# Kernel tuning notes

Hardware: AMD Instinct MI355X
Metric: run time of the kernel (lower is better)

Reference implementation:

```python
import jax, jax.numpy as jnp
import numpy as np
import math

D_MODEL = 2048
NUM_HEADS = 16
HEAD_DIM = D_MODEL // NUM_HEADS  # 128
B, S = 2, 2048


def setup_inputs() -> dict:
    key = jax.random.key(0)
    ks = jax.random.split(key, 11)
    s_in = 1.0 / math.sqrt(D_MODEL)
    return {
        "query": jax.random.normal(ks[0], (B, S, D_MODEL), dtype=jnp.float32),
        "key": jax.random.normal(ks[1], (B, S, D_MODEL), dtype=jnp.float32),
        "value": jax.random.normal(ks[2], (B, S, D_MODEL), dtype=jnp.float32),
        "Wq": jax.random.normal(ks[3], (D_MODEL, D_MODEL), dtype=jnp.float32) * s_in,
        "bq": jnp.zeros((D_MODEL,), dtype=jnp.float32),
        "Wk": jax.random.normal(ks[4], (D_MODEL, HEAD_DIM), dtype=jnp.float32) * s_in,
        "bk": jnp.zeros((HEAD_DIM,), dtype=jnp.float32),
        "Wv": jax.random.normal(ks[5], (D_MODEL, HEAD_DIM), dtype=jnp.float32) * s_in,
        "bv": jnp.zeros((HEAD_DIM,), dtype=jnp.float32),
        "Wo": jax.random.normal(ks[6], (D_MODEL, D_MODEL), dtype=jnp.float32) * s_in,
        "bo": jnp.zeros((D_MODEL,), dtype=jnp.float32),
    }


def reference(query, key, value, Wq, bq, Wk, bk, Wv, bv, Wo, bo):
    b, s, d_model = query.shape
    h, d = NUM_HEADS, HEAD_DIM
    # Projections: Q has h heads, K/V have a single shared head (MQA)
    Q = (query @ Wq + bq).reshape(b, s, h, d).transpose(0, 2, 1, 3)  # [b,h,s,d]
    K = key @ Wk + bk      # [b,s,d]
    V = value @ Wv + bv    # [b,s,d]
    scale = 1.0 / math.sqrt(d)
    # broadcast single K head over all h query heads
    scores = jnp.einsum('bhqd,bkd->bhqk', Q, K) * scale  # [b,h,s,s]
    weights = jax.nn.softmax(scores, axis=-1)
    attn = jnp.einsum('bhqk,bkd->bhqd', weights, V)      # [b,h,s,d]
    attn = attn.transpose(0, 2, 1, 3).reshape(b, s, d_model)
    return attn @ Wo + bo
```

## Files before the change

### kernel.cpp

```cpp
#include <hip/hip_runtime.h>


typedef unsigned short u16;
typedef __attribute__((ext_vector_type(8))) short bf16x8;
typedef __attribute__((ext_vector_type(4))) short bf16x4;
typedef __attribute__((ext_vector_type(4))) float f32x4;

#define D_MODEL 2048
#define SEQ     2048
#define NH      16
#define HD      128
#define BK      32

__device__ __forceinline__ u16 f2bf(float f){
  union { float f; unsigned u; } v; v.f = f;
  unsigned r = (v.u + 0x7FFFu + ((v.u >> 16) & 1u)) >> 16;
  return (u16)r;
}

#if __has_builtin(__builtin_amdgcn_cvt_pk_bf16_f32)
__device__ __forceinline__ unsigned pack2bf(float a, float b){
  auto v = __builtin_amdgcn_cvt_pk_bf16_f32(a, b);
  unsigned u; __builtin_memcpy(&u, &v, 4); return u;
}
#else
__device__ __forceinline__ unsigned pack2bf(float a, float b){
  return (unsigned)f2bf(a) | ((unsigned)f2bf(b) << 16);
}
#endif

__device__ __forceinline__ void gll16(const void* g, void* l){
  __builtin_amdgcn_global_load_lds(
      (const __attribute__((address_space(1))) void*)g,
      (__attribute__((address_space(3))) void*)l, 16, 0, 0);
}

__global__ __launch_bounds__(256) void prep_kernel(
    const float4* __restrict__ qa, const float4* __restrict__ ka, const float4* __restrict__ va,
    ushort4* __restrict__ oq, ushort4* __restrict__ ok, ushort4* __restrict__ ov,
    const float* __restrict__ Wq, const float* __restrict__ Wo,
    const float* __restrict__ Wk, const float* __restrict__ Wv,
    u16* __restrict__ WqT, u16* __restrict__ WoT,
    u16* __restrict__ WkT, u16* __restrict__ WvT){
  __shared__ float tt[32][33];
  int bid = blockIdx.x;
  if (bid < 8192){
    int i = bid*256 + threadIdx.x;
    float4 a = qa[i], b = ka[i], c = va[i];
    ushort4 ra, rb, rc;
    ra.x=f2bf(a.x); ra.y=f2bf(a.y); ra.z=f2bf(a.z); ra.w=f2bf(a.w);
    rb.x=f2bf(b.x); rb.y=f2bf(b.y); rb.z=f2bf(b.z); rb.w=f2bf(b.w);
    rc.x=f2bf(c.x); rc.y=f2bf(c.y); rc.z=f2bf(c.z); rc.w=f2bf(c.w);
    oq[i]=ra; ok[i]=rb; ov[i]=rc;
    return;
  }
  int id = bid - 8192;
  const float* in; u16* outp; int C, bx, by;
  if (id < 4096)      { in=Wq; outp=WqT; C=2048; bx=id&63;        by=id>>6; }
  else if (id < 8192) { id-=4096; in=Wo; outp=WoT; C=2048; bx=id&63; by=id>>6; }
  else if (id < 8448) { id-=8192; in=Wk; outp=WkT; C=128;  bx=id&3;  by=id>>2; }
  else                { id-=8448; in=Wv; outp=WvT; C=128;  bx=id&3;  by=id>>2; }
  const int R = 2048;
  int c0 = bx*32, r0 = by*32;
  int tx = threadIdx.x & 31, ty = threadIdx.x >> 5;
  #pragma unroll
  for (int k=0;k<4;k++) tt[ty+k*8][tx] = in[(size_t)(r0+ty+k*8)*C + c0+tx];
  __syncthreads();
  #pragma unroll
  for (int k=0;k<4;k++) outp[(size_t)(c0+ty+k*8)*R + r0+tx] = f2bf(tt[tx][ty+k*8]);
}

__device__ __forceinline__ void gemm_core_3p(
    const u16* __restrict__ A, const u16* __restrict__ BT,
    int lda, int ldb, int m0, int n0, int kbeg, int kend,
    u16* As, u16* Bs, f32x4 acc[4][4])
{
  const int t = threadIdx.x;
  const int w = t >> 6, l = t & 63;
  const int wr = w >> 1, wc = w & 1;
  const int c16 = l & 15, q = l >> 4;
  const int srow = l >> 2;
  const int sc   = ((l & 3) ^ ((l >> 3) & 3)) * 8;

  int aoff[4], boff[4];
  #pragma unroll
  for (int mt=0;mt<4;mt++){
    int row = wr*64 + mt*16 + c16;
    aoff[mt] = row*BK + ((q ^ ((row>>1)&3))*8);
  }
  #pragma unroll
  for (int nt=0;nt<4;nt++){
    int row = wc*64 + nt*16 + c16;
    boff[nt] = row*BK + ((q ^ ((row>>1)&3))*8);
  }

  auto issue = [&](int k0, int buf){
    u16* Ad = As + buf*4096;
    u16* Bd = Bs + buf*4096;
    #pragma unroll
    for (int half=0; half<2; half++){
      int r = half*64 + w*16 + srow;
      gll16(A  + (size_t)(m0+r)*lda + k0 + sc, Ad + (half*64 + w*16)*BK);
      gll16(BT + (size_t)(n0+r)*ldb + k0 + sc, Bd + (half*64 + w*16)*BK);
    }
  };

  const int n = (kend - kbeg) / BK;
  issue(kbeg, 0);
  issue(kbeg + BK, 1);
  int bi = 0;
  for (int i = 0; i < n; i++){
    if (i + 1 < n) asm volatile("s_waitcnt vmcnt(4)" ::: "memory");
    else           asm volatile("s_waitcnt vmcnt(0)" ::: "memory");
    __builtin_amdgcn_s_barrier();
    if (i + 2 < n){
      int nb = bi + 2; if (nb >= 3) nb -= 3;
      issue(kbeg + (i+2)*BK, nb);
    }
    const u16* Ab = As + bi*4096;
    const u16* Bb = Bs + bi*4096;
    bf16x8 af[4], bfr[4];
    #pragma unroll
    for (int mt=0;mt<4;mt++) af[mt]  = *(const bf16x8*)(Ab + aoff[mt]);
    #pragma unroll
    for (int nt=0;nt<4;nt++) bfr[nt] = *(const bf16x8*)(Bb + boff[nt]);
    #pragma unroll
    for (int mt=0;mt<4;mt++)
      #pragma unroll
      for (int nt=0;nt<4;nt++)
        acc[mt][nt] = __builtin_amdgcn_mfma_f32_16x16x32_bf16(af[mt], bfr[nt], acc[mt][nt], 0,0,0);
    bi++; if (bi == 3) bi = 0;
  }
}

__global__ __launch_bounds__(256) void proj_kernel(
    const u16* __restrict__ qb, const u16* __restrict__ kb, const u16* __restrict__ vb,
    const u16* __restrict__ WqT, const u16* __restrict__ WkT, const u16* __restrict__ WvT,
    const float* __restrict__ bq, u16* __restrict__ Qp, float* __restrict__ part)
{
  __shared__ u16 As[3*4096], Bs[3*4096];
  f32x4 acc[4][4];
  f32x4 z = {0.f,0.f,0.f,0.f};
  #pragma unroll
  for (int i=0;i<4;i++) for (int j=0;j<4;j++) acc[i][j] = z;
  const int t = threadIdx.x, w = t>>6, l = t&63, wr = w>>1, wc = w&1, c16 = l&15, q = l>>4;
  int id = blockIdx.x;
  if (id < 512){
    int x = id & 7, j = id >> 3;
    int m0 = (x*4 + (j & 3))*128, n0 = (j >> 2)*128;
    gemm_core_3p(qb, WqT, 2048, 2048, m0, n0, 0, 2048, As, Bs, acc);
    #pragma unroll
    for (int mt=0;mt<4;mt++)
      #pragma unroll
      for (int nt=0;nt<4;nt++){
        int col = n0 + wc*64 + nt*16 + c16;
        float bv = bq[col];
        #pragma unroll
        for (int r=0;r<4;r++){
          int row = m0 + wr*64 + mt*16 + q*4 + r;
          Qp[(size_t)row*D_MODEL + col] = f2bf(acc[mt][nt][r] + bv);
        }
      }
  } else {
    int kvid = id - 512;
    int zi = kvid & 3, nb = (kvid >> 2) & 1, mi = kvid >> 3;
    const u16* Am = nb ? vb  : kb;
    const u16* Bm = nb ? WvT : WkT;
    gemm_core_3p(Am, Bm, 2048, 2048, mi*128, 0, zi*512, zi*512+512, As, Bs, acc);
    float* dst = part + (size_t)(zi*2 + nb)*524288;
    #pragma unroll
    for (int mt=0;mt<4;mt++)
      #pragma unroll
      for (int nt=0;nt<4;nt++){
        int col = wc*64 + nt*16 + c16;
        #pragma unroll
        for (int r=0;r<4;r++){
          int row = mi*128 + wr*64 + mt*16 + q*4 + r;
          dst[(size_t)row*128 + col] = acc[mt][nt][r];
        }
      }
  }
}

__global__ __launch_bounds__(256) void oproj_kernel(
    const u16* __restrict__ A, const u16* __restrict__ BT, const float* __restrict__ bias,
    float* __restrict__ C)
{
  __shared__ u16 As[3*4096], Bs[3*4096];
  f32x4 acc[4][4];
  f32x4 z = {0.f,0.f,0.f,0.f};
  #pragma unroll
  for (int i=0;i<4;i++) for (int j=0;j<4;j++) acc[i][j] = z;
  int id = blockIdx.x;
  int x = id & 7, j = id >> 3;
  int m0 = (x*4 + (j & 3))*128, n0 = (j >> 2)*128;
  gemm_core_3p(A, BT, 2048, 2048, m0, n0, 0, 2048, As, Bs, acc);
  const int t = threadIdx.x, w = t>>6, l = t&63, wr = w>>1, wc = w&1, c16 = l&15, q = l>>4;
  #pragma unroll
  for (int mt=0;mt<4;mt++)
    #pragma unroll
    for (int nt=0;nt<4;nt++){
      int col = n0 + wc*64 + nt*16 + c16;
      float bv = bias[col];
      #pragma unroll
      for (int r=0;r<4;r++){
        int row = m0 + wr*64 + mt*16 + q*4 + r;
        C[(size_t)row*D_MODEL + col] = acc[mt][nt][r] + bv;
      }
    }
}

__global__ __launch_bounds__(256) void kv_reduce_kernel(
    const float* __restrict__ part, const float* __restrict__ bk, const float* __restrict__ bv,
    u16* __restrict__ Kp, u16* __restrict__ VpT){
  int idx = blockIdx.x*256 + threadIdx.x;
  int d = idx & 127, sg = idx >> 7;
  float ka = 0.f, va = 0.f;
  #pragma unroll
  for (int zi=0; zi<4; zi++){
    ka += part[(size_t)(zi*2+0)*524288 + idx];
    va += part[(size_t)(zi*2+1)*524288 + idx];
  }
  Kp[idx] = f2bf(ka + bk[d]);
  int b = sg >> 11, sl = sg & 2047;
  VpT[(size_t)b*262144 + (size_t)d*2048 + sl] = f2bf(va + bv[d]);
}

__global__ __launch_bounds__(512, 2) void attn_kernel(
    const u16* __restrict__ Qp, const u16* __restrict__ Kp,
    const u16* __restrict__ VpT, u16* __restrict__ attnb){
  __shared__ u16 lds[65536];
  const int t = threadIdx.x;
  const int w = t >> 6, l = t & 63;
  const int c16 = l & 15, q = l >> 4;

  const int qt = blockIdx.x;
  const int bh = blockIdx.y;
  const int b = bh >> 4, h = bh & 15;

  const u16* Qbase = Qp  + ((size_t)(b*SEQ + qt*256 + w*32))*D_MODEL + h*HD;
  const u16* Kbase = Kp  + (size_t)(b*SEQ)*HD;
  const u16* Vbase = VpT + (size_t)b*HD*SEQ;

  const int sr = w*4 + (l >> 4);
  #pragma unroll
  for (int j=0;j<4;j++){
    int r = j*32 + sr;
    int g = (l & 15) ^ (r & 15);
    gll16(Kbase + (size_t)r*HD + g*8, lds + j*4096 + w*512);
  }
  #pragma unroll
  for (int j=0;j<4;j++){
    int d = j*32 + sr;
    int g = (l & 15) ^ (d & 15);
    gll16(Vbase + (size_t)d*SEQ + g*8, lds + 32768 + j*4096 + w*512);
  }
  bf16x8 qf[2][4];
  #pragma unroll
  for (int qs=0;qs<2;qs++)
    #pragma unroll
    for (int kk=0;kk<4;kk++)
      qf[qs][kk] = *(const bf16x8*)(Qbase + (size_t)(qs*16 + c16)*D_MODEL + (kk*4 + q)*8);
  __syncthreads();

  f32x4 o[2][8];
  f32x4 z4 = {0.f,0.f,0.f,0.f};
  #pragma unroll
  for (int qs=0;qs<2;qs++) for (int dt=0;dt<8;dt++) o[qs][dt] = z4;
  float mrow[2] = {-1e30f, -1e30f};
  float lrow[2] = {0.f, 0.f};
  const float cs = 0.08838834764831845f * 1.4426950408889634f;

  for (int kt = 0; kt < 16; kt++){
    const int p = kt & 1;
    if (kt < 15){
      u16* Kd = lds + (p^1)*16384;
      u16* Vd = lds + 32768 + (p^1)*16384;
      #pragma unroll
      for (int j=0;j<4;j++){
        int r = j*32 + sr;
        int g = (l & 15) ^ (r & 15);
        gll16(Kbase + (size_t)((kt+1)*128 + r)*HD + g*8, Kd + j*4096 + w*512);
      }
      #pragma unroll
      for (int j=0;j<4;j++){
        int d = j*32 + sr;
        int g = (l & 15) ^ (d & 15);
        gll16(Vbase + (size_t)d*SEQ + (kt+1)*128 + g*8, Vd + j*4096 + w*512);
      }
    }
    const u16* Ks = lds + p*16384;
    const u16* Vs = lds + 32768 + p*16384;

    f32x4 s[2][8];
    __builtin_amdgcn_s_setprio(1);
    #pragma unroll
    for (int kt8=0; kt8<8; kt8++){
      {
        bf16x8 kf = *(const bf16x8*)(Ks + (kt8*16 + c16)*128 + ((q ^ c16) & 15)*8);
        s[0][kt8] = __builtin_amdgcn_mfma_f32_16x16x32_bf16(kf, qf[0][0], z4, 0,0,0);
        s[1][kt8] = __builtin_amdgcn_mfma_f32_16x16x32_bf16(kf, qf[1][0], z4, 0,0,0);
      }
      #pragma unroll
      for (int kk=1;kk<4;kk++){
        int ch = kk*4 + q;
        bf16x8 kf = *(const bf16x8*)(Ks + (kt8*16 + c16)*128 + ((ch ^ c16) & 15)*8);
        s[0][kt8] = __builtin_amdgcn_mfma_f32_16x16x32_bf16(kf, qf[0][kk], s[0][kt8], 0,0,0);
        s[1][kt8] = __builtin_amdgcn_mfma_f32_16x16x32_bf16(kf, qf[1][kk], s[1][kt8], 0,0,0);
      }
    }
    __builtin_amdgcn_s_setprio(0);

    float vmax[2];
    #pragma unroll
    for (int qs=0; qs<2; qs++){
      float xx[8];
      #pragma unroll
      for (int kt8=0;kt8<8;kt8++)
        xx[kt8] = fmaxf(fmaxf(s[qs][kt8][0],s[qs][kt8][1]), fmaxf(s[qs][kt8][2],s[qs][kt8][3]));
      float vm = fmaxf(fmaxf(fmaxf(xx[0],xx[1]),fmaxf(xx[2],xx[3])),
                       fmaxf(fmaxf(xx[4],xx[5]),fmaxf(xx[6],xx[7])));
      vm = fmaxf(vm, __shfl_xor(vm, 16));
      vm = fmaxf(vm, __shfl_xor(vm, 32));
      vmax[qs] = vm;
    }
    bool upd = ((vmax[0]-mrow[0])*cs > 8.f) || ((vmax[1]-mrow[1])*cs > 8.f);
    if (__any(upd)){
      #pragma unroll
      for (int qs=0; qs<2; qs++){
        float mnew = fmaxf(mrow[qs], vmax[qs]);
        float a = exp2f((mrow[qs]-mnew)*cs);
        mrow[qs] = mnew; lrow[qs] *= a;
        #pragma unroll
        for (int dt=0;dt<8;dt++)
          #pragma unroll
          for (int r=0;r<4;r++) o[qs][dt][r] *= a;
      }
    }
    union PU { unsigned u[4]; bf16x8 v; } P32[2][4];
    #pragma unroll
    for (int qs=0; qs<2; qs++){
      float mc = mrow[qs]*cs;
      float rsum = 0.f;
      #pragma unroll
      for (int kt8=0;kt8<8;kt8++){
        float p0 = exp2f(__builtin_fmaf(s[qs][kt8][0], cs, -mc));
        float p1 = exp2f(__builtin_fmaf(s[qs][kt8][1], cs, -mc));
        float p2 = exp2f(__builtin_fmaf(s[qs][kt8][2], cs, -mc));
        float p3 = exp2f(__builtin_fmaf(s[qs][kt8][3], cs, -mc));
        s[qs][kt8][0]=p0; s[qs][kt8][1]=p1; s[qs][kt8][2]=p2; s[qs][kt8][3]=p3;
        rsum += (p0+p1)+(p2+p3);
      }
      rsum += __shfl_xor(rsum, 16);
      rsum += __shfl_xor(rsum, 32);
      lrow[qs] += rsum;
      #pragma unroll
      for (int kb=0;kb<4;kb++){
        P32[qs][kb].u[0] = pack2bf(s[qs][2*kb][0],   s[qs][2*kb][1]);
        P32[qs][kb].u[1] = pack2bf(s[qs][2*kb][2],   s[qs][2*kb][3]);
        P32[qs][kb].u[2] = pack2bf(s[qs][2*kb+1][0], s[qs][2*kb+1][1]);
        P32[qs][kb].u[3] = pack2bf(s[qs][2*kb+1][2], s[qs][2*kb+1][3]);
      }
    }

    __builtin_amdgcn_s_setprio(1);
    #pragma unroll
    for (int kb=0; kb<4; kb++){
      int ca = 4*kb + (q>>1);
      int cb = ca + 2;
      #pragma unroll
      for (int dt=0; dt<8; dt++){
        int d = dt*16 + c16;
        union VU { bf16x4 hh[2]; bf16x8 v; } vf;
        vf.hh[0] = *(const bf16x4*)(Vs + d*128 + ((ca ^ c16) & 15)*8 + (q&1)*4);
        vf.hh[1] = *(const bf16x4*)(Vs + d*128 + ((cb ^ c16) & 15)*8 + (q&1)*4);
        o[0][dt] = __builtin_amdgcn_mfma_f32_16x16x32_bf16(vf.v, P32[0][kb].v, o[0][dt], 0,0,0);
        o[1][dt] = __builtin_amdgcn_mfma_f32_16x16x32_bf16(vf.v, P32[1][kb].v, o[1][dt], 0,0,0);
      }
    }
    __builtin_amdgcn_s_setprio(0);
    __syncthreads();
  }

  #pragma unroll
  for (int qs=0;qs<2;qs++){
    float inv = 1.f / lrow[qs];
    int qrow = qt*256 + w*32 + qs*16 + c16;
    u16* dst = attnb + ((size_t)(b*SEQ) + qrow)*D_MODEL + h*HD + q*4;
    #pragma unroll
    for (int dt=0;dt<8;dt++){
      ushort4 pk;
      pk.x = f2bf(o[qs][dt][0]*inv);
      pk.y = f2bf(o[qs][dt][1]*inv);
      pk.z = f2bf(o[qs][dt][2]*inv);
      pk.w = f2bf(o[qs][dt][3]*inv);
      *(ushort4*)(dst + dt*16) = pk;
    }
  }
}

extern "C" void kernel_launch(void* const* d_in, const int* in_sizes, int n_in,
                              void* d_out, int out_size, void* d_ws, size_t ws_size,
                              hipStream_t stream) {
  (void)in_sizes; (void)n_in; (void)out_size; (void)ws_size;
  const float* query = (const float*)d_in[0];
  const float* key   = (const float*)d_in[1];
  const float* value = (const float*)d_in[2];
  const float* Wq    = (const float*)d_in[3];
  const float* bq    = (const float*)d_in[4];
  const float* Wk    = (const float*)d_in[5];
  const float* bk    = (const float*)d_in[6];
  const float* Wv    = (const float*)d_in[7];
  const float* bv    = (const float*)d_in[8];
  const float* Wo    = (const float*)d_in[9];
  const float* bo    = (const float*)d_in[10];
  float* out = (float*)d_out;

  char* W = (char*)d_ws;
  u16*  qb     = (u16*) (W + 0);
  u16*  kb     = (u16*) (W + 16777216);
  u16*  vb     = (u16*) (W + 33554432);
  u16*  WqT    = (u16*) (W + 50331648);
  u16*  WoT    = (u16*) (W + 58720256);
  u16*  WkT    = (u16*) (W + 67108864);
  u16*  WvT    = (u16*) (W + 67633152);
  u16*  Qp     = (u16*) (W + 68157440);
  u16*  Kp     = (u16*) (W + 84934656);
  u16*  VpT    = (u16*) (W + 85983232);
  u16*  attnb  = (u16*) (W + 87031808);
  float* kvpart= (float*)(W + 103809024);

  prep_kernel<<<16896, 256, 0, stream>>>(
      (const float4*)query, (const float4*)key, (const float4*)value,
      (ushort4*)qb, (ushort4*)kb, (ushort4*)vb,
      Wq, Wo, Wk, Wv, WqT, WoT, WkT, WvT);
  proj_kernel<<<768, 256, 0, stream>>>(qb, kb, vb, WqT, WkT, WvT, bq, Qp, kvpart);
  kv_reduce_kernel<<<2048, 256, 0, stream>>>(kvpart, bk, bv, Kp, VpT);
  attn_kernel<<<dim3(8,32), 512, 0, stream>>>(Qp, Kp, VpT, attnb);
  oproj_kernel<<<512, 256, 0, stream>>>(attnb, WoT, bo, out);
}
```

Measured before the change: 404.3 us.

## Fuse Q projection into attention kernel prologue

Moves the Q projection GEMM out of proj_kernel and computes each 256x128 Q tile inside attn_kernel, staging it through LDS before the flash-attention loop. This removes the Qp global round-trip and the separate Q tiles in the projection launch. In exchange, the attention blocks do a full K=2048 GEMM prologue with only 256 blocks of 512 threads, which may lower GEMM efficiency versus the wider 512-block projection launch.

Measured after the change: 385.7 us. 4.6% less time.

```diff
diff --git a/kernel.cpp b/kernel.cpp
--- a/kernel.cpp
+++ b/kernel.cpp
@@ -134,9 +134,9 @@
 }
 
 __global__ __launch_bounds__(256) void proj_kernel(
-    const u16* __restrict__ qb, const u16* __restrict__ kb, const u16* __restrict__ vb,
-    const u16* __restrict__ WqT, const u16* __restrict__ WkT, const u16* __restrict__ WvT,
-    const float* __restrict__ bq, u16* __restrict__ Qp, float* __restrict__ part)
+    const u16* __restrict__ kb, const u16* __restrict__ vb,
+    const u16* __restrict__ WkT, const u16* __restrict__ WvT,
+    float* __restrict__ part)
 {
   __shared__ u16 As[3*4096], Bs[3*4096];
   f32x4 acc[4][4];
@@ -145,41 +145,22 @@
   for (int i=0;i<4;i++) for (int j=0;j<4;j++) acc[i][j] = z;
   const int t = threadIdx.x, w = t>>6, l = t&63, wr = w>>1, wc = w&1, c16 = l&15, q = l>>4;
   int id = blockIdx.x;
-  if (id < 512){
-    int x = id & 7, j = id >> 3;
-    int m0 = (x*4 + (j & 3))*128, n0 = (j >> 2)*128;
-    gemm_core_3p(qb, WqT, 2048, 2048, m0, n0, 0, 2048, As, Bs, acc);
-    #pragma unroll
-    for (int mt=0;mt<4;mt++)
-      #pragma unroll
-      for (int nt=0;nt<4;nt++){
-        int col = n0 + wc*64 + nt*16 + c16;
-        float bv = bq[col];
-        #pragma unroll
-        for (int r=0;r<4;r++){
-          int row = m0 + wr*64 + mt*16 + q*4 + r;
-          Qp[(size_t)row*D_MODEL + col] = f2bf(acc[mt][nt][r] + bv);
-        }
-      }
-  } else {
-    int kvid = id - 512;
-    int zi = kvid & 3, nb = (kvid >> 2) & 1, mi = kvid >> 3;
-    const u16* Am = nb ? vb  : kb;
-    const u16* Bm = nb ? WvT : WkT;
-    gemm_core_3p(Am, Bm, 2048, 2048, mi*128, 0, zi*512, zi*512+512, As, Bs, acc);
-    float* dst = part + (size_t)(zi*2 + nb)*524288;
-    #pragma unroll
-    for (int mt=0;mt<4;mt++)
-      #pragma unroll
-      for (int nt=0;nt<4;nt++){
-        int col = wc*64 + nt*16 + c16;
-        #pragma unroll
-        for (int r=0;r<4;r++){
-          int row = mi*128 + wr*64 + mt*16 + q*4 + r;
-          dst[(size_t)row*128 + col] = acc[mt][nt][r];
-        }
-      }
-  }
+  int zi = id & 3, nb = (id >> 2) & 1, mi = id >> 3;
+  const u16* Am = nb ? vb  : kb;
+  const u16* Bm = nb ? WvT : WkT;
+  gemm_core_3p(Am, Bm, 2048, 2048, mi*128, 0, zi*512, zi*512+512, As, Bs, acc);
+  float* dst = part + (size_t)(zi*2 + nb)*524288;
+  #pragma unroll
+  for (int mt=0;mt<4;mt++)
+    #pragma unroll
+    for (int nt=0;nt<4;nt++){
+      int col = wc*64 + nt*16 + c16;
+      #pragma unroll
+      for (int r=0;r<4;r++){
+        int row = mi*128 + wr*64 + mt*16 + q*4 + r;
+        dst[(size_t)row*128 + col] = acc[mt][nt][r];
+      }
+    }
 }
 
 __global__ __launch_bounds__(256) void oproj_kernel(
@@ -227,8 +208,8 @@
 }
 
 __global__ __launch_bounds__(512, 2) void attn_kernel(
-    const u16* __restrict__ Qp, const u16* __restrict__ Kp,
-    const u16* __restrict__ VpT, u16* __restrict__ attnb){
+    const u16* __restrict__ qb, const u16* __restrict__ WqT, const float* __restrict__ bq,
+    const u16* __restrict__ Kp, const u16* __restrict__ VpT, u16* __restrict__ attnb){
   __shared__ u16 lds[65536];
   const int t = threadIdx.x;
   const int w = t >> 6, l = t & 63;
@@ -238,10 +219,89 @@
   const int bh = blockIdx.y;
   const int b = bh >> 4, h = bh & 15;
 
-  const u16* Qbase = Qp  + ((size_t)(b*SEQ + qt*256 + w*32))*D_MODEL + h*HD;
+  f32x4 o[2][8];
+  f32x4 z4 = {0.f,0.f,0.f,0.f};
+  #pragma unroll
+  for (int qs=0;qs<2;qs++) for (int dt=0;dt<8;dt++) o[qs][dt] = z4;
+
+  {
+    const u16* Aq = qb  + (size_t)(b*SEQ + qt*256)*D_MODEL;
+    const u16* Bw = WqT + (size_t)(h*HD)*D_MODEL;
+    u16* As = lds;
+    u16* Bs = lds + 24576;
+    const int srow = l >> 2;
+    const int sc   = ((l & 3) ^ ((l >> 3) & 3)) * 8;
+    auto issueQ = [&](int k0, int buf){
+      u16* Ad = As + buf*8192;
+      u16* Bd = Bs + buf*4096;
+      #pragma unroll
+      for (int half=0; half<2; half++){
+        int r = half*128 + w*16 + srow;
+        gll16(Aq + (size_t)r*D_MODEL + k0 + sc, Ad + (half*128 + w*16)*BK);
+      }
+      { int r = w*16 + srow;
+        gll16(Bw + (size_t)r*D_MODEL + k0 + sc, Bd + (w*16)*BK); }
+    };
+    issueQ(0, 0);
+    issueQ(BK, 1);
+    int bi = 0;
+    const int swz = (q ^ ((c16>>1)&3))*8;
+    for (int i = 0; i < 64; i++){
+      if (i + 1 < 64) asm volatile("s_waitcnt vmcnt(3)" ::: "memory");
+      else            asm volatile("s_waitcnt vmcnt(0)" ::: "memory");
+      __builtin_amdgcn_s_barrier();
+      if (i + 2 < 64){
+        int nb2 = bi + 2; if (nb2 >= 3) nb2 -= 3;
+        issueQ((i+2)*BK, nb2);
+      }
+      const u16* Ab = As + bi*8192;
+      const u16* Bb = Bs + bi*4096;
+      bf16x8 qrow0 = *(const bf16x8*)(Ab + (w*32      + c16)*BK + swz);
+      bf16x8 qrow1 = *(const bf16x8*)(Ab + (w*32 + 16 + c16)*BK + swz);
+      bf16x8 wcol[8];
+      #pragma unroll
+      for (int dt=0;dt<8;dt++)
+        wcol[dt] = *(const bf16x8*)(Bb + (dt*16 + c16)*BK + swz);
+      __builtin_amdgcn_s_setprio(1);
+      #pragma unroll
+      for (int dt=0;dt<8;dt++){
+        o[0][dt] = __builtin_amdgcn_mfma_f32_16x16x32_bf16(wcol[dt], qrow0, o[0][dt], 0,0,0);
+        o[1][dt] = __builtin_amdgcn_mfma_f32_16x16x32_bf16(wcol[dt], qrow1, o[1][dt], 0,0,0);
+      }
+      __builtin_amdgcn_s_setprio(0);
+      bi++; if (bi == 3) bi = 0;
+    }
+    __syncthreads();
+    #pragma unroll
+    for (int qs=0;qs<2;qs++){
+      int row = w*32 + qs*16 + c16;
+      #pragma unroll
+      for (int dt=0;dt<8;dt++){
+        float4 bb = *(const float4*)(bq + h*HD + dt*16 + q*4);
+        uint2 val;
+        val.x = pack2bf(o[qs][dt][0]+bb.x, o[qs][dt][1]+bb.y);
+        val.y = pack2bf(o[qs][dt][2]+bb.z, o[qs][dt][3]+bb.w);
+        int ch = dt*2 + (q>>1);
+        *(uint2*)(lds + row*128 + ((ch ^ c16)&15)*8 + (q&1)*4) = val;
+      }
+    }
+    __syncthreads();
+  }
+
+  bf16x8 qf[2][4];
+  #pragma unroll
+  for (int qs=0;qs<2;qs++)
+    #pragma unroll
+    for (int kk=0;kk<4;kk++){
+      int ch = kk*4 + q;
+      qf[qs][kk] = *(const bf16x8*)(lds + (w*32 + qs*16 + c16)*128 + ((ch ^ c16)&15)*8);
+    }
+  __syncthreads();
+  #pragma unroll
+  for (int qs=0;qs<2;qs++) for (int dt=0;dt<8;dt++) o[qs][dt] = z4;
+
   const u16* Kbase = Kp  + (size_t)(b*SEQ)*HD;
   const u16* Vbase = VpT + (size_t)b*HD*SEQ;
-
   const int sr = w*4 + (l >> 4);
   #pragma unroll
   for (int j=0;j<4;j++){
@@ -255,18 +315,8 @@
     int g = (l & 15) ^ (d & 15);
     gll16(Vbase + (size_t)d*SEQ + g*8, lds + 32768 + j*4096 + w*512);
   }
-  bf16x8 qf[2][4];
-  #pragma unroll
-  for (int qs=0;qs<2;qs++)
-    #pragma unroll
-    for (int kk=0;kk<4;kk++)
-      qf[qs][kk] = *(const bf16x8*)(Qbase + (size_t)(qs*16 + c16)*D_MODEL + (kk*4 + q)*8);
   __syncthreads();
 
-  f32x4 o[2][8];
-  f32x4 z4 = {0.f,0.f,0.f,0.f};
-  #pragma unroll
-  for (int qs=0;qs<2;qs++) for (int dt=0;dt<8;dt++) o[qs][dt] = z4;
   float mrow[2] = {-1e30f, -1e30f};
   float lrow[2] = {0.f, 0.f};
   const float cs = 0.08838834764831845f * 1.4426950408889634f;
@@ -424,7 +474,6 @@
   u16*  WoT    = (u16*) (W + 58720256);
   u16*  WkT    = (u16*) (W + 67108864);
   u16*  WvT    = (u16*) (W + 67633152);
-  u16*  Qp     = (u16*) (W + 68157440);
   u16*  Kp     = (u16*) (W + 84934656);
   u16*  VpT    = (u16*) (W + 85983232);
   u16*  attnb  = (u16*) (W + 87031808);
@@ -434,8 +483,8 @@
       (const float4*)query, (const float4*)key, (const float4*)value,
       (ushort4*)qb, (ushort4*)kb, (ushort4*)vb,
       Wq, Wo, Wk, Wv, WqT, WoT, WkT, WvT);
-  proj_kernel<<<768, 256, 0, stream>>>(qb, kb, vb, WqT, WkT, WvT, bq, Qp, kvpart);
+  proj_kernel<<<256, 256, 0, stream>>>(kb, vb, WkT, WvT, kvpart);
   kv_reduce_kernel<<<2048, 256, 0, stream>>>(kvpart, bk, bv, Kp, VpT);
-  attn_kernel<<<dim3(8,32), 512, 0, stream>>>(Qp, Kp, VpT, attnb);
+  attn_kernel<<<dim3(8,32), 512, 0, stream>>>(qb, WqT, bq, Kp, VpT, attnb);
   oproj_kernel<<<512, 256, 0, stream>>>(attnb, WoT, bo, out);
 }
```
